# Kernel optimization log

Measured on AMD Instinct MI355X. Metric: run time of the kernel, lower is better.

## Reference

```python
import jax, jax.numpy as jnp
import numpy as np

B, S, D, H, F, L, V, SPAN = 4, 1024, 1024, 16, 4096, 4, 32000, 512
DH = D // H
NEG = -1e9


def _ln(x, g, b, eps=1e-12):
    m = x.mean(-1, keepdims=True)
    v = ((x - m) ** 2).mean(-1, keepdims=True)
    return (x - m) * jax.lax.rsqrt(v + eps) * g + b


def setup_inputs() -> dict:
    key = jax.random.key(0)
    ks = iter(jax.random.split(key, 40))
    g = lambda shape: jax.random.normal(next(ks), shape, jnp.float32) * 0.02
    inp = {
        "input_ids": jax.random.randint(next(ks), (B, S), 0, V),
        "segment_ids": jnp.zeros((B, S), jnp.int32),
        "attention_mask": jnp.ones((B, S), jnp.float32),
        "tok_emb": g((V, D)),
        "seg_emb": g((2, D)),
        "emb_ln_g": jnp.ones((D,), jnp.float32),
        "emb_ln_b": jnp.zeros((D,), jnp.float32),
        "rel_emb": g((2 * SPAN, D)),
        "Wq": g((L, D, D)), "bq": jnp.zeros((L, D), jnp.float32),
        "Wk": g((L, D, D)), "bk": jnp.zeros((L, D), jnp.float32),
        "Wv": g((L, D, D)), "bv": jnp.zeros((L, D), jnp.float32),
        "Wo": g((L, D, D)), "bo": jnp.zeros((L, D), jnp.float32),
        "ln1_g": jnp.ones((L, D), jnp.float32), "ln1_b": jnp.zeros((L, D), jnp.float32),
        "W1": g((L, D, F)), "b1": jnp.zeros((L, F), jnp.float32),
        "W2": g((L, F, D)), "b2": jnp.zeros((L, D), jnp.float32),
        "ln2_g": jnp.ones((L, D), jnp.float32), "ln2_b": jnp.zeros((L, D), jnp.float32),
    }
    return inp


def _forward(input_ids, segment_ids, attention_mask, tok_emb, seg_emb, emb_ln_g,
             emb_ln_b, rel_emb, Wq, bq, Wk, bk, Wv, bv, Wo, bo, ln1_g, ln1_b,
             W1, b1, W2, b2, ln2_g, ln2_b):
    # BertEmbedding (max_len=0 => no absolute positions): token + segment, LN, mask
    h = _ln(tok_emb[input_ids] + seg_emb[segment_ids], emb_ln_g, emb_ln_b)
    h = h * attention_mask[..., None]

    # relative positions (bucket_size=0 path): rel[q,k] = q - k, clamped into table
    pos = jnp.arange(S)
    rel = pos[:, None] - pos[None, :]                      # [S,S]
    c2p_idx = jnp.clip(rel + SPAN, 0, 2 * SPAN - 1)        # [S,S]
    p2c_idx = jnp.clip(-rel + SPAN, 0, 2 * SPAN - 1)       # [S,S]
    bias = (1.0 - attention_mask)[:, None, None, :] * NEG  # [B,1,1,S] additive mask

    scale = 1.0 / jnp.sqrt(jnp.asarray(DH * 3, h.dtype))   # scale_factor = 1 + |{c2p,p2c}|

    def layer(h, p):
        wq, bq_, wk, bk_, wv, bv_, wo, bo_, g1, b1n, w1, b1f, w2, b2f, g2, b2n = p
        q = (h @ wq + bq_).reshape(B, S, H, DH)
        k = (h @ wk + bk_).reshape(B, S, H, DH)
        v = (h @ wv + bv_).reshape(B, S, H, DH)
        att = jnp.einsum('bqhd,bkhd->bhqk', q, k) * scale
        # disentangled relative-position bias (shared q/k projections on rel table)
        pos_k = (rel_emb @ wk + bk_).reshape(2 * SPAN, H, DH)
        pos_q = (rel_emb @ wq + bq_).reshape(2 * SPAN, H, DH)
        c2p = jnp.einsum('bqhd,phd->bhqp', q, pos_k) * scale   # [B,H,S,2*SPAN]
        att = att + jnp.take_along_axis(c2p, c2p_idx[None, None], axis=-1)
        p2c = jnp.einsum('bkhd,phd->bhkp', k, pos_q) * scale   # [B,H,S,2*SPAN]
        att = att + jnp.swapaxes(
            jnp.take_along_axis(p2c, p2c_idx[None, None], axis=-1), -1, -2)
        probs = jax.nn.softmax(att + bias, axis=-1)
        ctx = jnp.einsum('bhqk,bkhd->bqhd', probs, v).reshape(B, S, D)
        h = _ln(h + ctx @ wo + bo_, g1, b1n)
        ff = jax.nn.gelu(h @ w1 + b1f, approximate=False) @ w2 + b2f
        return _ln(h + ff, g2, b2n), None

    h, _ = jax.lax.scan(layer, h, (Wq, bq, Wk, bk, Wv, bv, Wo, bo,
                                   ln1_g, ln1_b, W1, b1, W2, b2, ln2_g, ln2_b))
    return h


def reference(input_ids, segment_ids, attention_mask, tok_emb, seg_emb, emb_ln_g,
              emb_ln_b, rel_emb, Wq, bq, Wk, bk, Wv, bv, Wo, bo, ln1_g, ln1_b,
              W1, b1, W2, b2, ln2_g, ln2_b):
    return _forward(input_ids, segment_ids, attention_mask, tok_emb, seg_emb,
                    emb_ln_g, emb_ln_b, rel_emb, Wq, bq, Wk, bk, Wv, bv, Wo, bo,
                    ln1_g, ln1_b, W1, b1, W2, b2, ln2_g, ln2_b)
```

## Files before the change

### kernel.cpp

```cpp
#include <hip/hip_runtime.h>

#define DEV __device__ __forceinline__

typedef __bf16 bf16;
typedef __bf16 bf16x4 __attribute__((ext_vector_type(4)));
typedef __bf16 bf16x8 __attribute__((ext_vector_type(8)));
typedef float f32x4 __attribute__((ext_vector_type(4)));

constexpr int B_ = 4, S_ = 1024, D_ = 1024, H_ = 16, F_ = 4096, L_ = 4, SPAN_ = 512, DH_ = 64;
constexpr float SCALE_ = 0.07216878364870322f;
constexpr float LOG2E_ = 1.4426950408889634f;
constexpr float SCL2_ = SCALE_ * LOG2E_;

DEV void gload_lds16(const void* g, void* l) {
  __builtin_amdgcn_global_load_lds((const __attribute__((address_space(1))) void*)g,
                                   (__attribute__((address_space(3))) void*)l, 16, 0, 0);
}

template <int CTRL>
DEV float dppf(float x) {
  return __builtin_bit_cast(
      float, __builtin_amdgcn_mov_dpp(__builtin_bit_cast(int, x), CTRL, 0xf, 0xf, true));
}
DEV float rowMax16(float v) {
  v = fmaxf(v, dppf<0x128>(v));
  v = fmaxf(v, dppf<0x124>(v));
  v = fmaxf(v, dppf<0x122>(v));
  v = fmaxf(v, dppf<0x121>(v));
  return v;
}
DEV float rowSum16(float v) {
  v += dppf<0x128>(v);
  v += dppf<0x124>(v);
  v += dppf<0x122>(v);
  v += dppf<0x121>(v);
  return v;
}

DEV float blockSum4(float v, volatile float* red) {
#pragma unroll
  for (int o = 32; o; o >>= 1) v += __shfl_xor(v, o);
  if ((threadIdx.x & 63) == 0) red[threadIdx.x >> 6] = v;
  __syncthreads();
  return red[0] + red[1] + red[2] + red[3];
}

DEV bf16x8 lds_frag(const bf16* buf, int row, int chunk) {
  return *(const bf16x8*)((const char*)buf + row * 128 + ((chunk ^ (row & 7)) << 4));
}
DEV bf16x8 rdfrag(const char* base, int row, int chunk) {
  return *(const bf16x8*)(base + row * 128 + ((chunk ^ (row & 7)) << 4));
}

template <int EPI>
__global__ __launch_bounds__(512, 1) void gemm256(
    const bf16* __restrict__ A, const bf16* __restrict__ Bm,
    const float* __restrict__ bias, void* __restrict__ Cout,
    int K, int lda, int ldb, int ldc, long sA, long sB, long sC) {
  extern __shared__ __align__(16) char smem[];

  const int z = blockIdx.z;
  A += (long)z * sA;
  Bm += (long)z * sB;
  const long coff = (long)z * sC;

  const int nwg = gridDim.x * gridDim.y;
  const int flat = blockIdx.y * gridDim.x + blockIdx.x;
  const int qq = nwg >> 3;
  const int swz = (flat & 7) * qq + (flat >> 3);
  const int bx = swz % gridDim.x, by = swz / gridDim.x;
  const int m0 = by * 256, n0 = bx * 256;

  const int tid = threadIdx.x, lane = tid & 63, wave = tid >> 6;
  const int wr = wave >> 2, wc = wave & 3;
  const int fr = lane & 15, fq = lane >> 4;

  f32x4 acc[8][4];
#pragma unroll
  for (int m = 0; m < 8; m++)
#pragma unroll
    for (int n = 0; n < 4; n++) acc[m][n] = f32x4{0.f, 0.f, 0.f, 0.f};

  const int r8 = tid >> 3;
  const int swzel = ((tid & 7) ^ (r8 & 7)) << 3;
  const bf16* ga = A + (long)(m0 + r8) * lda + swzel;
  const bf16* gb = Bm + (long)(n0 + r8) * ldb + swzel;

  const int NT = K >> 6;

  auto stage = [&](int t) {
    const long ko = (long)t * 64;
    char* da = smem + ((t & 1) << 15) + wave * 1024;
    gload_lds16(ga + ko, da);
    gload_lds16(ga + 64 * (long)lda + ko, da + 8192);
    gload_lds16(ga + 128 * (long)lda + ko, da + 16384);
    gload_lds16(ga + 192 * (long)lda + ko, da + 24576);
    char* db = smem + 65536 + ((t & 1) << 15) + wave * 1024;
    gload_lds16(gb + ko, db);
    gload_lds16(gb + 64 * (long)ldb + ko, db + 8192);
    gload_lds16(gb + 128 * (long)ldb + ko, db + 16384);
    gload_lds16(gb + 192 * (long)ldb + ko, db + 24576);
  };

  stage(0);
  asm volatile("s_waitcnt vmcnt(0)" ::: "memory");
  __builtin_amdgcn_s_barrier();

  for (int j = 0; j < NT; j++) {
    const char* Ac = smem + ((j & 1) << 15);
    const char* Bc = smem + 65536 + ((j & 1) << 15);

    bf16x8 af[4][2], bfg[4][2];
#pragma unroll
    for (int m = 0; m < 4; m++) {
      const int ar = wr * 128 + m * 16 + fr;
      af[m][0] = rdfrag(Ac, ar, fq);
      af[m][1] = rdfrag(Ac, ar, 4 + fq);
    }
#pragma unroll
    for (int n = 0; n < 4; n++) {
      const int br = wc * 64 + n * 16 + fr;
      bfg[n][0] = rdfrag(Bc, br, fq);
      bfg[n][1] = rdfrag(Bc, br, 4 + fq);
    }
    if (j + 1 < NT) stage(j + 1);

    __builtin_amdgcn_s_setprio(1);
#pragma unroll
    for (int m = 0; m < 4; m++)
#pragma unroll
      for (int n = 0; n < 4; n++)
#pragma unroll
        for (int kc = 0; kc < 2; kc++)
          acc[m][n] = __builtin_amdgcn_mfma_f32_16x16x32_bf16(af[m][kc], bfg[n][kc],
                                                              acc[m][n], 0, 0, 0);
    __builtin_amdgcn_s_setprio(0);
    __builtin_amdgcn_sched_barrier(0);

#pragma unroll
    for (int m = 0; m < 4; m++) {
      const int ar = wr * 128 + (m + 4) * 16 + fr;
      af[m][0] = rdfrag(Ac, ar, fq);
      af[m][1] = rdfrag(Ac, ar, 4 + fq);
    }
    __builtin_amdgcn_s_setprio(1);
#pragma unroll
    for (int m = 0; m < 4; m++)
#pragma unroll
      for (int n = 0; n < 4; n++)
#pragma unroll
        for (int kc = 0; kc < 2; kc++)
          acc[m + 4][n] = __builtin_amdgcn_mfma_f32_16x16x32_bf16(af[m][kc], bfg[n][kc],
                                                                  acc[m + 4][n], 0, 0, 0);
    __builtin_amdgcn_s_setprio(0);

    asm volatile("s_waitcnt vmcnt(0)" ::: "memory");
    __builtin_amdgcn_s_barrier();
  }

#pragma unroll
  for (int m = 0; m < 8; m++) {
#pragma unroll
    for (int n = 0; n < 4; n++) {
      const int col = n0 + wc * 64 + n * 16 + fr;
      float bval = 0.f;
      if constexpr (EPI == 3 || EPI == 4) bval = bias ? bias[col] : 0.f;
#pragma unroll
      for (int rr = 0; rr < 4; rr++) {
        const int row = m0 + wr * 128 + m * 16 + fq * 4 + rr;
        const long idx = coff + (long)row * ldc + col;
        const float v = acc[m][n][rr];
        if constexpr (EPI == 0) ((float*)Cout)[idx] = v;
        else if constexpr (EPI == 3) ((bf16*)Cout)[idx] = (bf16)(v + bval);
        else if constexpr (EPI == 4) {
          float x = v + bval;
          x = 0.5f * x * (1.f + erff(x * 0.70710678118654752f));
          ((bf16*)Cout)[idx] = (bf16)x;
        }
      }
    }
  }
}

template <int EPI>
__global__ __launch_bounds__(256) void gemm_bt(
    const bf16* __restrict__ A, const bf16* __restrict__ Bm,
    const float* __restrict__ bias, void* __restrict__ Cout,
    int M, int N, int K, int lda, int ldb, int ldc, float alpha,
    long sA, long sB, long sC) {
  __shared__ alignas(16) bf16 As[128 * 64];
  __shared__ alignas(16) bf16 Bs[128 * 64];

  const int z = blockIdx.z;
  A += (long)z * sA;
  Bm += (long)z * sB;
  const long coff = (long)z * sC;

  const int nwg = gridDim.x * gridDim.y;
  const int flat = blockIdx.y * gridDim.x + blockIdx.x;
  const int qq = nwg >> 3;
  const int swz = (flat & 7) * qq + (flat >> 3);
  const int bx = swz % gridDim.x, by = swz / gridDim.x;

  const int m0 = by * 128, n0 = bx * 128;
  const int tid = threadIdx.x, lane = tid & 63, wave = tid >> 6;
  const int wr = wave >> 1, wc = wave & 1;
  const int fr = lane & 15, fq = lane >> 4;

  f32x4 acc[4][4];
#pragma unroll
  for (int m = 0; m < 4; m++)
#pragma unroll
    for (int n = 0; n < 4; n++) acc[m][n] = f32x4{0.f, 0.f, 0.f, 0.f};

  const int r8 = tid >> 3;
  const int swzel = ((tid & 7) ^ (r8 & 7)) << 3;
  const bf16* ga = A + (long)(m0 + r8) * lda + swzel;
  const bf16* gb = Bm + (long)(n0 + r8) * ldb + swzel;
  const int swzrd = fr & 7;

  for (int k0 = 0; k0 < K; k0 += 64) {
#pragma unroll
    for (int i = 0; i < 4; i++)
      gload_lds16(ga + (long)i * 32 * lda + k0, (char*)As + i * 4096 + wave * 1024);
#pragma unroll
    for (int i = 0; i < 4; i++)
      gload_lds16(gb + (long)i * 32 * ldb + k0, (char*)Bs + i * 4096 + wave * 1024);
    __syncthreads();
#pragma unroll
    for (int kc = 0; kc < 2; kc++) {
      bf16x8 af[4], bfv[4];
#pragma unroll
      for (int m = 0; m < 4; m++)
        af[m] = *(const bf16x8*)((char*)As + (wr * 64 + m * 16 + fr) * 128 +
                                 (((kc * 4 + fq) ^ swzrd) << 4));
#pragma unroll
      for (int n = 0; n < 4; n++)
        bfv[n] = *(const bf16x8*)((char*)Bs + (wc * 64 + n * 16 + fr) * 128 +
                                  (((kc * 4 + fq) ^ swzrd) << 4));
#pragma unroll
      for (int m = 0; m < 4; m++)
#pragma unroll
        for (int n = 0; n < 4; n++)
          acc[m][n] = __builtin_amdgcn_mfma_f32_16x16x32_bf16(af[m], bfv[n], acc[m][n], 0, 0, 0);
    }
    __syncthreads();
  }

#pragma unroll
  for (int m = 0; m < 4; m++) {
#pragma unroll
    for (int n = 0; n < 4; n++) {
      const int col = n0 + wc * 64 + n * 16 + fr;
      float bval = 0.f;
      if constexpr (EPI == 3 || EPI == 4 || EPI == 5) bval = bias ? bias[col] : 0.f;
#pragma unroll
      for (int rr = 0; rr < 4; rr++) {
        const int row = m0 + wr * 64 + m * 16 + fq * 4 + rr;
        const long idx = coff + (long)row * ldc + col;
        const float v = acc[m][n][rr];
        if constexpr (EPI == 0) ((float*)Cout)[idx] = v * alpha;
        else if constexpr (EPI == 3) ((bf16*)Cout)[idx] = (bf16)(v + bval);
        else if constexpr (EPI == 4) {
          float x = v + bval;
          x = 0.5f * x * (1.f + erff(x * 0.70710678118654752f));
          ((bf16*)Cout)[idx] = (bf16)x;
        } else if constexpr (EPI == 5) {
          const long pidx = ((long)(col >> 6) * 1024 + row) * 64 + (col & 63);
          ((bf16*)Cout)[pidx] = (bf16)(v + bval);
        }
      }
    }
  }
}

__global__ __launch_bounds__(256) void repack_kv(const bf16* __restrict__ qkv,
                                                 bf16* __restrict__ kp,
                                                 bf16* __restrict__ vp) {
  const int kt = blockIdx.x, bh = blockIdx.y;
  const int b = bh >> 4, h = bh & 15;
  const int k0 = kt * 64;
  __shared__ bf16 t[64][72];
  const int ty = threadIdx.x >> 3, tx = threadIdx.x & 7;
#pragma unroll
  for (int p = 0; p < 2; p++) {
    const int s = k0 + p * 32 + ty;
    const long base = (long)(b * 1024 + s) * 3072 + h * 64;
    bf16x8 kv = *(const bf16x8*)(qkv + base + 1024 + tx * 8);
    *(bf16x8*)(kp + ((long)(bh * 1024 + s) << 6) + tx * 8) = kv;
    bf16x8 vv = *(const bf16x8*)(qkv + base + 2048 + tx * 8);
    *(bf16x8*)(&t[p * 32 + ty][tx * 8]) = vv;
  }
  __syncthreads();
  const int dh = threadIdx.x >> 2, sc = (threadIdx.x & 3) * 16;
  bf16 tmp[16];
#pragma unroll
  for (int j = 0; j < 16; j++) tmp[j] = t[sc + j][dh];
  bf16* dst = vp + ((long)(bh * 16 + kt) << 12) + dh * 64 + sc;
  *(bf16x8*)dst = *(bf16x8*)tmp;
  *(bf16x8*)(dst + 8) = *(bf16x8*)(tmp + 8);
}

__global__ __launch_bounds__(256) void attn_fused(
    const bf16* __restrict__ qkv, const bf16* __restrict__ kp,
    const bf16* __restrict__ vp, const bf16* __restrict__ pospk,
    const float* __restrict__ mask, bf16* __restrict__ ctx) {
  const int id = blockIdx.x;
  const int xcd = id & 7, sub = id >> 3;
  const int bh = xcd + 8 * (sub >> 4);
  const int qt = sub & 15;
  const int b = bh >> 4, h = bh & 15;
  const int q0 = qt * 64;
  const int tid = threadIdx.x, wave = tid >> 6, lane = tid & 63;
  const int fr = lane & 15, fq = lane >> 4;

  __shared__ alignas(16) char smem[61952];
  bf16* PXk = (bf16*)smem;
  bf16* p2c_T = (bf16*)smem;
  bf16* Ks = (bf16*)(smem + 16384);
  bf16* PXq = (bf16*)(smem + 24576);
  char* p_l = smem + 24576;
  bf16* Vs = (bf16*)(smem + 40960);
  bf16* c2p_T = (bf16*)(smem + 49152);

  const bf16* posq = pospk + ((long)h << 16);
  const bf16* posk = pospk + ((long)(16 + h) << 16);
  const bf16* kbase = kp + ((long)bh << 16);
  const bf16* vbase = vp + ((long)bh << 16);

  bf16x8 qa[2];
  {
    const bf16* qrow = qkv + (long)(b * 1024 + q0 + wave * 16 + fr) * 3072 + h * 64;
    qa[0] = *(const bf16x8*)(qrow + fq * 8);
    qa[1] = *(const bf16x8*)(qrow + 32 + fq * 8);
  }

  f32x4 o[4];
#pragma unroll
  for (int n = 0; n < 4; n++) o[n] = f32x4{0.f, 0.f, 0.f, 0.f};
  float m_r[4], l_r[4];
#pragma unroll
  for (int r = 0; r < 4; r++) { m_r[r] = -1e30f; l_r[r] = 0.f; }

  char* pl_base = p_l + wave * 2048;
  bf16* c2p_w = c2p_T + wave * 1600;
  const int wbyte = wave * 1024;

  for (int kt = 0; kt < 16; kt++) {
    const int k0 = kt * 64;

    __syncthreads();
    {
      const int j0k = q0 - k0 + 449;
      const int j0q = k0 - q0 + 449;
#pragma unroll
      for (int c = 0; c < 4; c++) {
        const int u = c * 256 + tid;
        const int rr = u >> 3;
        const int sel = (((u & 7) ^ (rr & 7)) << 3);
        int jk = j0k + rr;
        jk = jk < 0 ? 0 : (jk > 1023 ? 1023 : jk);
        gload_lds16(posk + ((long)jk << 6) + sel, (char*)PXk + c * 4096 + wbyte);
        int jq = j0q + rr;
        jq = jq < 0 ? 0 : (jq > 1023 ? 1023 : jq);
        gload_lds16(posq + ((long)jq << 6) + sel, (char*)PXq + c * 4096 + wbyte);
      }
#pragma unroll
      for (int c = 0; c < 2; c++) {
        const int u = c * 256 + tid;
        const int rr = u >> 3;
        const int sel = (((u & 7) ^ (rr & 7)) << 3);
        gload_lds16(kbase + ((long)(k0 + rr) << 6) + sel, (char*)Ks + c * 4096 + wbyte);
        gload_lds16(vbase + ((long)kt << 12) + ((long)rr << 6) + sel,
                    (char*)Vs + c * 4096 + wbyte);
      }
    }
    __syncthreads();

    bf16x8 ka[2];
    ka[0] = lds_frag(Ks, wave * 16 + fr, fq);
    ka[1] = lds_frag(Ks, wave * 16 + fr, 4 + fq);
    {
      f32x4 cw[5];
#pragma unroll
      for (int t = 0; t < 5; t++) cw[t] = f32x4{0.f, 0.f, 0.f, 0.f};
#pragma unroll
      for (int kc = 0; kc < 2; kc++)
#pragma unroll
        for (int t = 0; t < 5; t++) {
          const bf16x8 pb = lds_frag(PXk, wave * 16 + t * 16 + fr, kc * 4 + fq);
          cw[t] = __builtin_amdgcn_mfma_f32_16x16x32_bf16(qa[kc], pb, cw[t], 0, 0, 0);
        }
#pragma unroll
      for (int t = 0; t < 5; t++) {
        bf16x4 pk;
#pragma unroll
        for (int r = 0; r < 4; r++) pk[r] = (bf16)cw[t][r];
        *(bf16x4*)&c2p_w[(t * 16 + fr) * 20 + fq * 4] = pk;
      }
    }
    f32x4 s[4];
#pragma unroll
    for (int n = 0; n < 4; n++) s[n] = f32x4{0.f, 0.f, 0.f, 0.f};
#pragma unroll
    for (int kc = 0; kc < 2; kc++)
#pragma unroll
      for (int n = 0; n < 4; n++) {
        const bf16x8 kb = lds_frag(Ks, n * 16 + fr, kc * 4 + fq);
        s[n] = __builtin_amdgcn_mfma_f32_16x16x32_bf16(qa[kc], kb, s[n], 0, 0, 0);
      }
    __syncthreads();

    {
      f32x4 pw[5];
#pragma unroll
      for (int t = 0; t < 5; t++) pw[t] = f32x4{0.f, 0.f, 0.f, 0.f};
#pragma unroll
      for (int kc = 0; kc < 2; kc++)
#pragma unroll
        for (int t = 0; t < 5; t++) {
          const bf16x8 pb = lds_frag(PXq, (wave + t) * 16 + fr, kc * 4 + fq);
          pw[t] = __builtin_amdgcn_mfma_f32_16x16x32_bf16(ka[kc], pb, pw[t], 0, 0, 0);
        }
#pragma unroll
      for (int t = 0; t < 5; t++) {
        bf16x4 pk;
#pragma unroll
        for (int r = 0; r < 4; r++) pk[r] = (bf16)pw[t][r];
        *(bf16x4*)&p2c_T[((wave + t) * 16 + fr) * 68 + wave * 16 + fq * 4] = pk;
      }
    }
    __syncthreads();

    bf16x8 vb[2][4];
#pragma unroll
    for (int kc = 0; kc < 2; kc++)
#pragma unroll
      for (int n = 0; n < 4; n++) vb[kc][n] = lds_frag(Vs, n * 16 + fr, kc * 4 + fq);

    float st[4][4];
#pragma unroll
    for (int n = 0; n < 4; n++) {
      const int ki = n * 16 + fr;
      const float mb = (1.0f - mask[b * S_ + k0 + ki]) * (-1e9f * LOG2E_);
#pragma unroll
      for (int r = 0; r < 4; r++) {
        const int qi_s = fq * 4 + r;
        const float cv = (float)c2p_w[(qi_s - ki + 63) * 20 + qi_s];
        const float pv = (float)p2c_T[(ki - (wave * 16 + qi_s) + 63) * 68 + ki];
        st[n][r] = (s[n][r] + cv + pv) * SCL2_ + mb;
      }
    }

    float sc[4];
#pragma unroll
    for (int r = 0; r < 4; r++) {
      float v = fmaxf(fmaxf(st[0][r], st[1][r]), fmaxf(st[2][r], st[3][r]));
      v = rowMax16(v);
      const float mn = fmaxf(m_r[r], v);
      sc[r] = exp2f(m_r[r] - mn);
      m_r[r] = mn;
    }
    float rs[4] = {0.f, 0.f, 0.f, 0.f};
#pragma unroll
    for (int n = 0; n < 4; n++) {
      const int ki = n * 16 + fr;
#pragma unroll
      for (int r = 0; r < 4; r++) {
        const int qi_s = fq * 4 + r;
        const float p = exp2f(st[n][r] - m_r[r]);
        rs[r] += p;
        *(bf16*)(pl_base + qi_s * 128 + ((ki * 2) ^ ((qi_s & 7) << 4))) = (bf16)p;
      }
    }
#pragma unroll
    for (int r = 0; r < 4; r++) {
      const float v = rowSum16(rs[r]);
      l_r[r] = l_r[r] * sc[r] + v;
#pragma unroll
      for (int n = 0; n < 4; n++) o[n][r] *= sc[r];
    }

#pragma unroll
    for (int kc = 0; kc < 2; kc++) {
      const bf16x8 pa =
          *(const bf16x8*)(pl_base + fr * 128 + ((kc * 64 + fq * 16) ^ ((fr & 7) << 4)));
#pragma unroll
      for (int n = 0; n < 4; n++)
        o[n] = __builtin_amdgcn_mfma_f32_16x16x32_bf16(pa, vb[kc][n], o[n], 0, 0, 0);
    }
  }

#pragma unroll
  for (int r = 0; r < 4; r++) {
    const float inv = 1.f / l_r[r];
    const long row = (long)(b * S_ + q0 + wave * 16 + fq * 4 + r) * D_ + h * 64;
#pragma unroll
    for (int n = 0; n < 4; n++) ctx[row + n * 16 + fr] = (bf16)(o[n][r] * inv);
  }
}

__global__ __launch_bounds__(256) void wtrans(const float* __restrict__ W,
                                              bf16* __restrict__ WT, int K, int N,
                                              long sW, long sT) {
  W += (long)blockIdx.z * sW;
  WT += (long)blockIdx.z * sT;
  __shared__ float t[32][33];
  const int n0 = blockIdx.x * 32, k0 = blockIdx.y * 32;
  const int tx = threadIdx.x & 31, ty = threadIdx.x >> 5;
#pragma unroll
  for (int i = ty; i < 32; i += 8) t[i][tx] = W[(long)(k0 + i) * N + n0 + tx];
  __syncthreads();
#pragma unroll
  for (int i = ty; i < 32; i += 8) WT[(long)(n0 + i) * K + k0 + tx] = (bf16)t[tx][i];
}

__global__ __launch_bounds__(256) void f2b(const float* __restrict__ in,
                                           bf16* __restrict__ out, long n) {
  long i = (long)blockIdx.x * 256 + threadIdx.x;
  if (i < n) out[i] = (bf16)in[i];
}

__global__ __launch_bounds__(256) void bias_concat(const float* __restrict__ bq,
                                                   const float* __restrict__ bk,
                                                   const float* __restrict__ bv,
                                                   float* __restrict__ bqkv) {
  const int i = blockIdx.x * 256 + threadIdx.x;
  const int l = i / (3 * D_), s = (i % (3 * D_)) / D_, d = i % D_;
  const float* src = s == 0 ? bq : (s == 1 ? bk : bv);
  bqkv[i] = src[l * D_ + d];
}

__global__ __launch_bounds__(256) void embed_ln(
    const int* __restrict__ ids, const int* __restrict__ segs,
    const float* __restrict__ mask, const float* __restrict__ tok,
    const float* __restrict__ seg, const float* __restrict__ g,
    const float* __restrict__ bta, float* __restrict__ h, bf16* __restrict__ hb) {
  __shared__ float r1[4], r2[4];
  const int t = blockIdx.x;
  const long tb = (long)ids[t] * D_;
  const long sb = (long)segs[t] * D_;
  const long base = (long)t * D_;
  float x[4];
  float sm = 0.f;
#pragma unroll
  for (int i = 0; i < 4; i++) {
    const int d = threadIdx.x + i * 256;
    x[i] = tok[tb + d] + seg[sb + d];
    sm += x[i];
  }
  sm = blockSum4(sm, r1);
  const float mean = sm * (1.f / D_);
  float vs = 0.f;
#pragma unroll
  for (int i = 0; i < 4; i++) {
    const float c = x[i] - mean;
    vs += c * c;
  }
  vs = blockSum4(vs, r2);
  const float rstd = rsqrtf(vs * (1.f / D_) + 1e-12f);
  const float mk = mask[t];
#pragma unroll
  for (int i = 0; i < 4; i++) {
    const int d = threadIdx.x + i * 256;
    const float y = ((x[i] - mean) * rstd * g[d] + bta[d]) * mk;
    h[base + d] = y;
    hb[base + d] = (bf16)y;
  }
}

template <int P>
__global__ __launch_bounds__(256) void ln_residual_red(
    const float* __restrict__ hin, float* __restrict__ hout,
    const float* __restrict__ part, long pstride,
    const float* __restrict__ bias, const float* __restrict__ g,
    const float* __restrict__ bta, bf16* __restrict__ hb) {
  __shared__ float r1[4], r2[4];
  const long base = (long)blockIdx.x * D_;
  float x[4];
  float sm = 0.f;
#pragma unroll
  for (int i = 0; i < 4; i++) {
    const int d = threadIdx.x + i * 256;
    float v = hin[base + d] + bias[d];
#pragma unroll
    for (int z = 0; z < P; z++) v += part[(long)z * pstride + base + d];
    x[i] = v;
    sm += v;
  }
  sm = blockSum4(sm, r1);
  const float mean = sm * (1.f / D_);
  float vs = 0.f;
#pragma unroll
  for (int i = 0; i < 4; i++) {
    const float c = x[i] - mean;
    vs += c * c;
  }
  vs = blockSum4(vs, r2);
  const float rstd = rsqrtf(vs * (1.f / D_) + 1e-12f);
#pragma unroll
  for (int i = 0; i < 4; i++) {
    const int d = threadIdx.x + i * 256;
    const float y = (x[i] - mean) * rstd * g[d] + bta[d];
    hout[base + d] = y;
    hb[base + d] = (bf16)y;
  }
}

extern "C" void kernel_launch(void* const* d_in, const int* in_sizes, int n_in,
                              void* d_out, int out_size, void* d_ws, size_t ws_size,
                              hipStream_t stream) {
  (void)in_sizes; (void)n_in; (void)out_size; (void)ws_size;
  const int* input_ids = (const int*)d_in[0];
  const int* segment_ids = (const int*)d_in[1];
  const float* attention_mask = (const float*)d_in[2];
  const float* tok_emb = (const float*)d_in[3];
  const float* seg_emb = (const float*)d_in[4];
  const float* emb_ln_g = (const float*)d_in[5];
  const float* emb_ln_b = (const float*)d_in[6];
  const float* rel_emb = (const float*)d_in[7];
  const float* Wq = (const float*)d_in[8];
  const float* bq = (const float*)d_in[9];
  const float* Wk = (const float*)d_in[10];
  const float* bk = (const float*)d_in[11];
  const float* Wv = (const float*)d_in[12];
  const float* bv = (const float*)d_in[13];
  const float* Wo = (const float*)d_in[14];
  const float* bo = (const float*)d_in[15];
  const float* ln1_g = (const float*)d_in[16];
  const float* ln1_b = (const float*)d_in[17];
  const float* W1 = (const float*)d_in[18];
  const float* b1 = (const float*)d_in[19];
  const float* W2 = (const float*)d_in[20];
  const float* b2 = (const float*)d_in[21];
  const float* ln2_g = (const float*)d_in[22];
  const float* ln2_b = (const float*)d_in[23];

  const long DD = (long)D_ * D_;
  const long DF = (long)D_ * F_;
  const int D3 = 3 * D_;

  char* ws = (char*)d_ws;
  auto alloc = [&](size_t bytes) {
    char* p = ws;
    ws += (bytes + 255) & ~(size_t)255;
    return p;
  };
  bf16* wqkvT = (bf16*)alloc((size_t)L_ * 3 * DD * 2);
  bf16* woT = (bf16*)alloc((size_t)L_ * DD * 2);
  bf16* w1T = (bf16*)alloc((size_t)L_ * DF * 2);
  bf16* w2T = (bf16*)alloc((size_t)L_ * DF * 2);
  float* bqkv = (float*)alloc((size_t)L_ * 3 * D_ * 4);
  bf16* relb = (bf16*)alloc((size_t)2 * SPAN_ * D_ * 2);
  float* hbuf = (float*)alloc((size_t)B_ * S_ * D_ * 4);
  bf16* hb = (bf16*)alloc((size_t)B_ * S_ * D_ * 2);
  bf16* qkv = (bf16*)alloc((size_t)B_ * S_ * 3 * D_ * 2);
  bf16* kp = (bf16*)alloc((size_t)B_ * H_ * S_ * DH_ * 2);
  bf16* vp = (bf16*)alloc((size_t)B_ * H_ * S_ * DH_ * 2);
  bf16* pospk = (bf16*)alloc((size_t)32 * 1024 * 64 * 2);
  bf16* ctxb = (bf16*)alloc((size_t)B_ * S_ * D_ * 2);
  bf16* ff1b = (bf16*)alloc((size_t)B_ * S_ * F_ * 2);
  float* kpart = (float*)alloc((size_t)4 * B_ * S_ * D_ * 4);
  const long PSTR = (long)B_ * S_ * D_;

  wtrans<<<dim3(D_ / 32, D_ / 32, L_), 256, 0, stream>>>(Wq, wqkvT + 0 * DD, D_, D_, DD, 3 * DD);
  wtrans<<<dim3(D_ / 32, D_ / 32, L_), 256, 0, stream>>>(Wk, wqkvT + 1 * DD, D_, D_, DD, 3 * DD);
  wtrans<<<dim3(D_ / 32, D_ / 32, L_), 256, 0, stream>>>(Wv, wqkvT + 2 * DD, D_, D_, DD, 3 * DD);
  wtrans<<<dim3(D_ / 32, D_ / 32, L_), 256, 0, stream>>>(Wo, woT, D_, D_, DD, DD);
  wtrans<<<dim3(F_ / 32, D_ / 32, L_), 256, 0, stream>>>(W1, w1T, D_, F_, DF, DF);
  wtrans<<<dim3(D_ / 32, F_ / 32, L_), 256, 0, stream>>>(W2, w2T, F_, D_, DF, DF);
  bias_concat<<<dim3(L_ * 3 * D_ / 256), 256, 0, stream>>>(bq, bk, bv, bqkv);
  f2b<<<dim3((2 * SPAN_ * D_) / 256), 256, 0, stream>>>(rel_emb, relb, (long)2 * SPAN_ * D_);
  embed_ln<<<dim3(B_ * S_), 256, 0, stream>>>(input_ids, segment_ids, attention_mask,
                                              tok_emb, seg_emb, emb_ln_g, emb_ln_b, hbuf, hb);

  const size_t SH = 131072;

  for (int l = 0; l < L_; ++l) {
    const bf16* wqkv_ = wqkvT + (long)l * 3 * DD;
    const bf16* wo_ = woT + (long)l * DD;
    const bf16* w1_ = w1T + (long)l * DF;
    const bf16* w2_ = w2T + (long)l * DF;
    const float* bqkv_ = bqkv + (long)l * 3 * D_;
    const float* bo_ = bo + (long)l * D_;
    const float* b1_ = b1 + (long)l * F_;
    const float* b2_ = b2 + (long)l * D_;

    gemm_bt<5><<<dim3((2 * D_) / 128, (2 * SPAN_) / 128, 1), 256, 0, stream>>>(
        relb, wqkv_, bqkv_, pospk, 2 * SPAN_, 2 * D_, D_, D_, D_, 0, 1.f, 0, 0, 0);

    gemm256<3><<<dim3(D3 / 256, (B_ * S_) / 256, 1), 512, SH, stream>>>(
        hb, wqkv_, bqkv_, qkv, D_, D_, D_, D3, 0, 0, 0);
    repack_kv<<<dim3(16, B_ * H_), 256, 0, stream>>>(qkv, kp, vp);

    attn_fused<<<dim3(1024), 256, 0, stream>>>(qkv, kp, vp, pospk, attention_mask, ctxb);

    gemm256<0><<<dim3(D_ / 256, (B_ * S_) / 256, 4), 512, SH, stream>>>(
        ctxb, wo_, nullptr, kpart, D_ / 4, D_, D_, D_, D_ / 4, D_ / 4, PSTR);
    ln_residual_red<4><<<dim3(B_ * S_), 256, 0, stream>>>(
        hbuf, hbuf, kpart, PSTR, bo_, ln1_g + l * D_, ln1_b + l * D_, hb);

    gemm256<4><<<dim3(F_ / 256, (B_ * S_) / 256, 1), 512, SH, stream>>>(
        hb, w1_, b1_, ff1b, D_, D_, D_, F_, 0, 0, 0);
    gemm256<0><<<dim3(D_ / 256, (B_ * S_) / 256, 4), 512, SH, stream>>>(
        ff1b, w2_, nullptr, kpart, F_ / 4, F_, F_, D_, F_ / 4, F_ / 4, PSTR);
    float* hout = (l == L_ - 1) ? (float*)d_out : hbuf;
    ln_residual_red<4><<<dim3(B_ * S_), 256, 0, stream>>>(
        hbuf, hout, kpart, PSTR, b2_, ln2_g + l * D_, ln2_b + l * D_, hb);
  }
}
```

Baseline: 1.513 ms.

## Batch rel-pos projections across layers, vectorize LN kernels, issue loads earlier

The per-layer relative-position projection GEMM is hoisted out of the layer loop into a single batched launch over all layers, using a z-dimension with per-layer bias and output strides. This removes three small launches and gives the GEMM a larger grid, at the cost of a bigger position buffer. The embedding and residual LayerNorm kernels now use float4 loads and stores with a packed bf16x4 write. The gemm256 loop also issues the next tile's global-to-LDS stage before reading fragments from the current buffer, to overlap global loads with LDS reads.

```diff
diff --git a/kernel.cpp b/kernel.cpp
--- a/kernel.cpp
+++ b/kernel.cpp
@@ -11,6 +11,7 @@
 constexpr float SCALE_ = 0.07216878364870322f;
 constexpr float LOG2E_ = 1.4426950408889634f;
 constexpr float SCL2_ = SCALE_ * LOG2E_;
+constexpr long POSL_ = 32L * 1024 * 64;
 
 DEV void gload_lds16(const void* g, void* l) {
   __builtin_amdgcn_global_load_lds((const __attribute__((address_space(1))) void*)g,
@@ -110,6 +111,8 @@
     const char* Ac = smem + ((j & 1) << 15);
     const char* Bc = smem + 65536 + ((j & 1) << 15);
 
+    if (j + 1 < NT) stage(j + 1);
+
     bf16x8 af[4][2], bfg[4][2];
 #pragma unroll
     for (int m = 0; m < 4; m++) {
@@ -123,7 +126,6 @@
       bfg[n][0] = rdfrag(Bc, br, fq);
       bfg[n][1] = rdfrag(Bc, br, 4 + fq);
     }
-    if (j + 1 < NT) stage(j + 1);
 
     __builtin_amdgcn_s_setprio(1);
 #pragma unroll
@@ -187,13 +189,14 @@
     const bf16* __restrict__ A, const bf16* __restrict__ Bm,
     const float* __restrict__ bias, void* __restrict__ Cout,
     int M, int N, int K, int lda, int ldb, int ldc, float alpha,
-    long sA, long sB, long sC) {
+    long sA, long sB, long sC, long sBias) {
   __shared__ alignas(16) bf16 As[128 * 64];
   __shared__ alignas(16) bf16 Bs[128 * 64];
 
   const int z = blockIdx.z;
   A += (long)z * sA;
   Bm += (long)z * sB;
+  bias += (long)z * sBias;
   const long coff = (long)z * sC;
 
   const int nwg = gridDim.x * gridDim.y;
@@ -266,7 +269,7 @@
           x = 0.5f * x * (1.f + erff(x * 0.70710678118654752f));
           ((bf16*)Cout)[idx] = (bf16)x;
         } else if constexpr (EPI == 5) {
-          const long pidx = ((long)(col >> 6) * 1024 + row) * 64 + (col & 63);
+          const long pidx = coff + ((long)(col >> 6) * 1024 + row) * 64 + (col & 63);
           ((bf16*)Cout)[pidx] = (bf16)(v + bval);
         }
       }
@@ -538,73 +541,80 @@
     const float* __restrict__ bta, float* __restrict__ h, bf16* __restrict__ hb) {
   __shared__ float r1[4], r2[4];
   const int t = blockIdx.x;
-  const long tb = (long)ids[t] * D_;
-  const long sb = (long)segs[t] * D_;
-  const long base = (long)t * D_;
-  float x[4];
-  float sm = 0.f;
-#pragma unroll
-  for (int i = 0; i < 4; i++) {
-    const int d = threadIdx.x + i * 256;
-    x[i] = tok[tb + d] + seg[sb + d];
-    sm += x[i];
-  }
+  const int d4 = threadIdx.x;
+  const long tb4 = (long)ids[t] * 256;
+  const long sb4 = (long)segs[t] * 256;
+  const long b4 = (long)t * 256;
+  f32x4 x = ((const f32x4*)tok)[tb4 + d4];
+  const f32x4 sv = ((const f32x4*)seg)[sb4 + d4];
+#pragma unroll
+  for (int r = 0; r < 4; r++) x[r] += sv[r];
+  float sm = x[0] + x[1] + x[2] + x[3];
   sm = blockSum4(sm, r1);
   const float mean = sm * (1.f / D_);
   float vs = 0.f;
 #pragma unroll
-  for (int i = 0; i < 4; i++) {
-    const float c = x[i] - mean;
+  for (int r = 0; r < 4; r++) {
+    const float c = x[r] - mean;
     vs += c * c;
   }
   vs = blockSum4(vs, r2);
   const float rstd = rsqrtf(vs * (1.f / D_) + 1e-12f);
   const float mk = mask[t];
-#pragma unroll
-  for (int i = 0; i < 4; i++) {
-    const int d = threadIdx.x + i * 256;
-    const float y = ((x[i] - mean) * rstd * g[d] + bta[d]) * mk;
-    h[base + d] = y;
-    hb[base + d] = (bf16)y;
-  }
+  const f32x4 gv = ((const f32x4*)g)[d4];
+  const f32x4 bv = ((const f32x4*)bta)[d4];
+  f32x4 y;
+  bf16x4 yb;
+#pragma unroll
+  for (int r = 0; r < 4; r++) {
+    y[r] = ((x[r] - mean) * rstd * gv[r] + bv[r]) * mk;
+    yb[r] = (bf16)y[r];
+  }
+  ((f32x4*)h)[b4 + d4] = y;
+  *(bf16x4*)&hb[(b4 + d4) * 4] = yb;
 }
 
 template <int P>
 __global__ __launch_bounds__(256) void ln_residual_red(
     const float* __restrict__ hin, float* __restrict__ hout,
-    const float* __restrict__ part, long pstride,
+    const float* __restrict__ part, long pstride4,
     const float* __restrict__ bias, const float* __restrict__ g,
     const float* __restrict__ bta, bf16* __restrict__ hb) {
   __shared__ float r1[4], r2[4];
-  const long base = (long)blockIdx.x * D_;
-  float x[4];
-  float sm = 0.f;
-#pragma unroll
-  for (int i = 0; i < 4; i++) {
-    const int d = threadIdx.x + i * 256;
-    float v = hin[base + d] + bias[d];
-#pragma unroll
-    for (int z = 0; z < P; z++) v += part[(long)z * pstride + base + d];
-    x[i] = v;
-    sm += v;
-  }
+  const int d4 = threadIdx.x;
+  const long b4 = (long)blockIdx.x * 256;
+  f32x4 x = ((const f32x4*)hin)[b4 + d4];
+  const f32x4 bi = ((const f32x4*)bias)[d4];
+#pragma unroll
+  for (int r = 0; r < 4; r++) x[r] += bi[r];
+#pragma unroll
+  for (int z = 0; z < P; z++) {
+    const f32x4 pv = ((const f32x4*)part)[(long)z * pstride4 + b4 + d4];
+#pragma unroll
+    for (int r = 0; r < 4; r++) x[r] += pv[r];
+  }
+  float sm = x[0] + x[1] + x[2] + x[3];
   sm = blockSum4(sm, r1);
   const float mean = sm * (1.f / D_);
   float vs = 0.f;
 #pragma unroll
-  for (int i = 0; i < 4; i++) {
-    const float c = x[i] - mean;
+  for (int r = 0; r < 4; r++) {
+    const float c = x[r] - mean;
     vs += c * c;
   }
   vs = blockSum4(vs, r2);
   const float rstd = rsqrtf(vs * (1.f / D_) + 1e-12f);
-#pragma unroll
-  for (int i = 0; i < 4; i++) {
-    const int d = threadIdx.x + i * 256;
-    const float y = (x[i] - mean) * rstd * g[d] + bta[d];
-    hout[base + d] = y;
-    hb[base + d] = (bf16)y;
-  }
+  const f32x4 gv = ((const f32x4*)g)[d4];
+  const f32x4 bv = ((const f32x4*)bta)[d4];
+  f32x4 y;
+  bf16x4 yb;
+#pragma unroll
+  for (int r = 0; r < 4; r++) {
+    y[r] = (x[r] - mean) * rstd * gv[r] + bv[r];
+    yb[r] = (bf16)y[r];
+  }
+  ((f32x4*)hout)[b4 + d4] = y;
+  *(bf16x4*)&hb[(b4 + d4) * 4] = yb;
 }
 
 extern "C" void kernel_launch(void* const* d_in, const int* in_sizes, int n_in,
@@ -657,7 +667,7 @@
   bf16* qkv = (bf16*)alloc((size_t)B_ * S_ * 3 * D_ * 2);
   bf16* kp = (bf16*)alloc((size_t)B_ * H_ * S_ * DH_ * 2);
   bf16* vp = (bf16*)alloc((size_t)B_ * H_ * S_ * DH_ * 2);
-  bf16* pospk = (bf16*)alloc((size_t)32 * 1024 * 64 * 2);
+  bf16* pospk = (bf16*)alloc((size_t)L_ * POSL_ * 2);
   bf16* ctxb = (bf16*)alloc((size_t)B_ * S_ * D_ * 2);
   bf16* ff1b = (bf16*)alloc((size_t)B_ * S_ * F_ * 2);
   float* kpart = (float*)alloc((size_t)4 * B_ * S_ * D_ * 4);
@@ -671,6 +681,9 @@
   wtrans<<<dim3(D_ / 32, F_ / 32, L_), 256, 0, stream>>>(W2, w2T, F_, D_, DF, DF);
   bias_concat<<<dim3(L_ * 3 * D_ / 256), 256, 0, stream>>>(bq, bk, bv, bqkv);
   f2b<<<dim3((2 * SPAN_ * D_) / 256), 256, 0, stream>>>(rel_emb, relb, (long)2 * SPAN_ * D_);
+  gemm_bt<5><<<dim3((2 * D_) / 128, (2 * SPAN_) / 128, L_), 256, 0, stream>>>(
+      relb, wqkvT, bqkv, pospk, 2 * SPAN_, 2 * D_, D_, D_, D_, 0, 1.f,
+      0, 3 * DD, POSL_, 3 * D_);
   embed_ln<<<dim3(B_ * S_), 256, 0, stream>>>(input_ids, segment_ids, attention_mask,
                                               tok_emb, seg_emb, emb_ln_g, emb_ln_b, hbuf, hb);
 
@@ -686,19 +699,17 @@
     const float* b1_ = b1 + (long)l * F_;
     const float* b2_ = b2 + (long)l * D_;
 
-    gemm_bt<5><<<dim3((2 * D_) / 128, (2 * SPAN_) / 128, 1), 256, 0, stream>>>(
-        relb, wqkv_, bqkv_, pospk, 2 * SPAN_, 2 * D_, D_, D_, D_, 0, 1.f, 0, 0, 0);
-
     gemm256<3><<<dim3(D3 / 256, (B_ * S_) / 256, 1), 512, SH, stream>>>(
         hb, wqkv_, bqkv_, qkv, D_, D_, D_, D3, 0, 0, 0);
     repack_kv<<<dim3(16, B_ * H_), 256, 0, stream>>>(qkv, kp, vp);
 
-    attn_fused<<<dim3(1024), 256, 0, stream>>>(qkv, kp, vp, pospk, attention_mask, ctxb);
+    attn_fused<<<dim3(1024), 256, 0, stream>>>(qkv, kp, vp, pospk + (long)l * POSL_,
+                                               attention_mask, ctxb);
 
     gemm256<0><<<dim3(D_ / 256, (B_ * S_) / 256, 4), 512, SH, stream>>>(
         ctxb, wo_, nullptr, kpart, D_ / 4, D_, D_, D_, D_ / 4, D_ / 4, PSTR);
     ln_residual_red<4><<<dim3(B_ * S_), 256, 0, stream>>>(
-        hbuf, hbuf, kpart, PSTR, bo_, ln1_g + l * D_, ln1_b + l * D_, hb);
+        hbuf, hbuf, kpart, PSTR / 4, bo_, ln1_g + l * D_, ln1_b + l * D_, hb);
 
     gemm256<4><<<dim3(F_ / 256, (B_ * S_) / 256, 1), 512, SH, stream>>>(
         hb, w1_, b1_, ff1b, D_, D_, D_, F_, 0, 0, 0);
@@ -706,6 +717,6 @@
         ff1b, w2_, nullptr, kpart, F_ / 4, F_, F_, D_, F_ / 4, F_ / 4, PSTR);
     float* hout = (l == L_ - 1) ? (float*)d_out : hbuf;
     ln_residual_red<4><<<dim3(B_ * S_), 256, 0, stream>>>(
-        hbuf, hout, kpart, PSTR, b2_, ln2_g + l * D_, ln2_b + l * D_, hb);
-  }
-}
+        hbuf, hout, kpart, PSTR / 4, b2_, ln2_g + l * D_, ln2_b + l * D_, hb);
+  }
+}
```

Measured after the change: 1.433 ms. 5.3% less time.
